# Optimization experiments

Measured on AMD Instinct MI355X. Metric: run time of the kernel, lower is better.

## Reference

```python
import jax, jax.numpy as jnp
import numpy as np

EPS = 0.1      # torchsort regularization_strength
OUTPUTS = 16   # GlobalMultimaxPool1d(outputs=16)


def _pav_decreasing(y):
    """Non-increasing isotonic regression (pool-adjacent-violators) on a 1-D array."""
    n = y.shape[0]

    def push(carry, yi):
        sums, counts, top = carry
        top = top + 1
        sums = sums.at[top].set(yi)
        counts = counts.at[top].set(1.0)

        def cond(st):
            s, c, t = st
            # mean(top) > mean(top-1)  <=>  s[t]*c[t-1] > s[t-1]*c[t]
            return (t > 0) & (s[t] * c[t - 1] > s[t - 1] * c[t])

        def merge(st):
            s, c, t = st
            s = s.at[t - 1].add(s[t]).at[t].set(0.0)
            c = c.at[t - 1].add(c[t]).at[t].set(0.0)
            return s, c, t - 1

        sums, counts, top = jax.lax.while_loop(cond, merge, (sums, counts, top))
        return (sums, counts, top), None

    init = (jnp.zeros(n, y.dtype), jnp.zeros(n, y.dtype), jnp.int32(-1))
    (sums, counts, _), _ = jax.lax.scan(push, init, y)
    means = sums / jnp.maximum(counts, 1.0)
    ends = jnp.cumsum(counts)                                 # block end offsets
    block = jnp.searchsorted(ends, jnp.arange(n) + 0.5)       # block id per position
    return means[block]


def _pav_rows(y):
    flat = y.reshape(-1, y.shape[-1])
    return jax.vmap(_pav_decreasing)(flat).reshape(y.shape)


@jax.custom_vjp
def isotonic_decreasing(y):
    return _pav_rows(y)


def _iso_fwd(y):
    v = _pav_rows(y)
    return v, v


def _iso_bwd(v, g):
    # Jacobian of PAV solution w.r.t. input is block-averaging within pooled blocks
    # (same analytic gradient torchsort uses).
    n = v.shape[-1]

    def row(vr, gr):
        new = jnp.concatenate([jnp.ones((1,), bool), vr[1:] != vr[:-1]])
        bid = jnp.cumsum(new) - 1
        s = jax.ops.segment_sum(gr, bid, num_segments=n)
        c = jax.ops.segment_sum(jnp.ones_like(gr), bid, num_segments=n)
        return (s / jnp.maximum(c, 1.0))[bid]

    gy = jax.vmap(row)(v.reshape(-1, n), g.reshape(-1, n)).reshape(v.shape)
    return (gy,)


isotonic_decreasing.defvjp(_iso_fwd, _iso_bwd)


def soft_sort(x, eps=EPS):
    """fast-soft-sort / torchsort l2 soft sort (ascending) along the last axis.

    sign=-1 (ascending): values=-x, sort descending -> s = -sort(x),
    res = isotonic_decreasing(w - s), output = -(w - res).
    """
    n = x.shape[-1]
    w = jnp.arange(n, 0, -1, dtype=x.dtype) / eps   # [n, n-1, ..., 1] / eps
    s = -jnp.sort(x, axis=-1)                        # descending sort of -x
    v = isotonic_decreasing(w - s)
    return -(w - v)


def setup_inputs() -> dict:
    key = jax.random.key(0)
    x = jax.random.normal(key, (16, 256, 2048), dtype=jnp.float32)
    return {"x": x}


def reference(x):
    z = soft_sort(x)                                  # (B, C, N) soft-ascending
    idx = z.shape[-1] - jnp.arange(OUTPUTS) - 1       # [N-1, N-2, ..., N-OUTPUTS]
    return jnp.take(z, idx, axis=-1)                  # (B, C, OUTPUTS)
```

## Files before the change

### kernel.cpp

```cpp
#include <hip/hip_runtime.h>
#include <math.h>


#define ROW_N 2048
#define K 16

__device__ __forceinline__ void ce_desc(float& a, float& b) {
    float mx = fmaxf(a, b);
    float mn = fminf(a, b);
    a = mx; b = mn;
}

__device__ __forceinline__ void sort16_desc(float* s) {
    #pragma unroll
    for (int k = 2; k <= 16; k <<= 1) {
        #pragma unroll
        for (int j = k >> 1; j > 0; j >>= 1) {
            #pragma unroll
            for (int i = 0; i < 16; ++i) {
                int l = i ^ j;
                if (l > i) {
                    if ((i & k) == 0) ce_desc(s[i], s[l]);
                    else              ce_desc(s[l], s[i]);
                }
            }
        }
    }
}

__device__ __forceinline__ void resort16_desc(float* s) {
    #pragma unroll
    for (int j = 8; j > 0; j >>= 1) {
        #pragma unroll
        for (int i = 0; i < 16; ++i) {
            int l = i ^ j;
            if (l > i) ce_desc(s[i], s[l]);
        }
    }
}

__global__ __launch_bounds__(256) void topk16_rows_kernel(
        const float* __restrict__ x, float* __restrict__ out, int nrows) {
    const int lane = threadIdx.x & 63;
    const int wid  = threadIdx.x >> 6;
    const int row  = blockIdx.x * 4 + wid;
    if (row >= nrows) return;

    const float4* rp4 = (const float4*)(x + (size_t)row * ROW_N);

    float a[16], b[16];
    #pragma unroll
    for (int j = 0; j < 4; ++j) {
        float4 t = rp4[lane + 64 * j];
        a[4 * j + 0] = t.x; a[4 * j + 1] = t.y;
        a[4 * j + 2] = t.z; a[4 * j + 3] = t.w;
    }
    #pragma unroll
    for (int j = 0; j < 4; ++j) {
        float4 t = rp4[lane + 64 * (j + 4)];
        b[4 * j + 0] = t.x; b[4 * j + 1] = t.y;
        b[4 * j + 2] = t.z; b[4 * j + 3] = t.w;
    }

    sort16_desc(a);
    sort16_desc(b);
    float t[16];
    #pragma unroll
    for (int i = 0; i < 16; ++i) t[i] = fmaxf(a[i], b[15 - i]);
    resort16_desc(t);

    #pragma unroll
    for (int st = 0; st < 6; ++st) {
        const int off = 1 << st;
        float p[16];
        #pragma unroll
        for (int i = 0; i < 16; ++i) p[i] = __shfl_xor(t[i], off, 64);
        float u[16];
        #pragma unroll
        for (int i = 0; i < 16; ++i) u[i] = fmaxf(t[i], p[15 - i]);
        resort16_desc(u);
        #pragma unroll
        for (int i = 0; i < 16; ++i) t[i] = u[i];
    }

    float myout = 0.0f;
    #pragma unroll
    for (int k = 0; k < K; ++k)
        if (lane == k) myout = t[k];
    if (lane < K) out[(size_t)row * K + lane] = myout;
}

extern "C" void kernel_launch(void* const* d_in, const int* in_sizes, int n_in,
                              void* d_out, int out_size, void* d_ws, size_t ws_size,
                              hipStream_t stream) {
    const float* x = (const float*)d_in[0];
    float* out = (float*)d_out;
    const int nrows = in_sizes[0] / ROW_N;
    const int blocks = (nrows + 3) / 4;
    topk16_rows_kernel<<<blocks, 256, 0, stream>>>(x, out, nrows);
}
```

Baseline: 15.23 us.

## Split each row across two wavefronts and merge top-16 via shared memory

Each 2048-element row is now handled by two wavefronts, each loading and sorting half the row (16 values per lane). The two per-wave top-16 lists are combined through shared memory with a bitonic merge done by shuffles. This doubles the number of waves to improve latency hiding and memory parallelism, and halves per-thread registers. It adds a __syncthreads and a small shared-memory merge, and the launch bounds now request 8 waves per EU occupancy.

```diff
diff --git a/kernel.cpp b/kernel.cpp
--- a/kernel.cpp
+++ b/kernel.cpp
@@ -2,8 +2,9 @@
 #include <math.h>
 
 
-#define ROW_N 2048
-#define K 16
+#define ROW_N  2048
+#define HALF_N 1024
+#define K      16
 
 __device__ __forceinline__ void ce_desc(float& a, float& b) {
     float mx = fmaxf(a, b);
@@ -39,55 +40,64 @@
     }
 }
 
-__global__ __launch_bounds__(256) void topk16_rows_kernel(
+__global__ __launch_bounds__(256, 8) void topk16_split_kernel(
         const float* __restrict__ x, float* __restrict__ out, int nrows) {
     const int lane = threadIdx.x & 63;
     const int wid  = threadIdx.x >> 6;
-    const int row  = blockIdx.x * 4 + wid;
-    if (row >= nrows) return;
+    const int gw   = blockIdx.x * 4 + wid;
+    int row        = gw >> 1;
+    const int half = gw & 1;
+    const bool valid = (row < nrows);
+    if (!valid) row = nrows - 1;
 
-    const float4* rp4 = (const float4*)(x + (size_t)row * ROW_N);
+    const float4* rp4 =
+        (const float4*)(x + (size_t)row * ROW_N + half * HALF_N);
 
-    float a[16], b[16];
+    float t[16];
     #pragma unroll
     for (int j = 0; j < 4; ++j) {
-        float4 t = rp4[lane + 64 * j];
-        a[4 * j + 0] = t.x; a[4 * j + 1] = t.y;
-        a[4 * j + 2] = t.z; a[4 * j + 3] = t.w;
-    }
-    #pragma unroll
-    for (int j = 0; j < 4; ++j) {
-        float4 t = rp4[lane + 64 * (j + 4)];
-        b[4 * j + 0] = t.x; b[4 * j + 1] = t.y;
-        b[4 * j + 2] = t.z; b[4 * j + 3] = t.w;
+        float4 v = rp4[lane + 64 * j];
+        t[4 * j + 0] = v.x; t[4 * j + 1] = v.y;
+        t[4 * j + 2] = v.z; t[4 * j + 3] = v.w;
     }
 
-    sort16_desc(a);
-    sort16_desc(b);
-    float t[16];
-    #pragma unroll
-    for (int i = 0; i < 16; ++i) t[i] = fmaxf(a[i], b[15 - i]);
-    resort16_desc(t);
+    sort16_desc(t);
 
     #pragma unroll
     for (int st = 0; st < 6; ++st) {
         const int off = 1 << st;
-        float p[16];
-        #pragma unroll
-        for (int i = 0; i < 16; ++i) p[i] = __shfl_xor(t[i], off, 64);
         float u[16];
         #pragma unroll
-        for (int i = 0; i < 16; ++i) u[i] = fmaxf(t[i], p[15 - i]);
+        for (int i = 0; i < 8; ++i) {
+            float pi = __shfl_xor(t[i], off, 64);
+            float pj = __shfl_xor(t[15 - i], off, 64);
+            u[i]      = fmaxf(t[i],      pj);
+            u[15 - i] = fmaxf(t[15 - i], pi);
+        }
         resort16_desc(u);
         #pragma unroll
         for (int i = 0; i < 16; ++i) t[i] = u[i];
     }
 
-    float myout = 0.0f;
+    float my = 0.0f;
     #pragma unroll
     for (int k = 0; k < K; ++k)
-        if (lane == k) myout = t[k];
-    if (lane < K) out[(size_t)row * K + lane] = myout;
+        if (lane == k) my = t[k];
+
+    __shared__ float sm[4][K];
+    if (lane < K) sm[wid][lane] = my;
+    __syncthreads();
+
+    if ((half == 0) && (lane < K)) {
+        float b = sm[wid ^ 1][(K - 1) - lane];
+        float m = fmaxf(my, b);
+        #pragma unroll
+        for (int j = 8; j >= 1; j >>= 1) {
+            float pm = __shfl_xor(m, j, 64);
+            m = ((lane & j) == 0) ? fmaxf(m, pm) : fminf(m, pm);
+        }
+        if (valid) out[(size_t)row * K + lane] = m;
+    }
 }
 
 extern "C" void kernel_launch(void* const* d_in, const int* in_sizes, int n_in,
@@ -95,7 +105,8 @@
                               hipStream_t stream) {
     const float* x = (const float*)d_in[0];
     float* out = (float*)d_out;
-    const int nrows = in_sizes[0] / ROW_N;
-    const int blocks = (nrows + 3) / 4;
-    topk16_rows_kernel<<<blocks, 256, 0, stream>>>(x, out, nrows);
+    const int nrows  = in_sizes[0] / ROW_N;
+    const int nwaves = nrows * 2;
+    const int blocks = (nwaves + 3) / 4;
+    topk16_split_kernel<<<blocks, 256, 0, stream>>>(x, out, nrows);
 }
```

Result: slower. 19.25 us (+26.4%).

## Prefilter candidates above a fixed threshold, then sort small candidate sets per row

Applied to the files above, without the earlier changes.

Replaces the full per-row bitonic top-16 with a three-pass scheme. Counters are zeroed, then a filter kernel uses ballot and atomics to gather elements above a fixed threshold into a 64-slot buffer per row. A select kernel finishes with a 64-lane shuffle sort, or falls back to the full path when the count is out of range. The goal is to avoid heavy register sorting networks, at the cost of extra launches, atomics, workspace traffic, and a threshold tuned to normally distributed inputs.

```diff
diff --git a/kernel.cpp b/kernel.cpp
--- a/kernel.cpp
+++ b/kernel.cpp
@@ -4,6 +4,9 @@
 
 #define ROW_N 2048
 #define K 16
+#define CAP 64
+#define THRESH 2.05f
+
 
 __device__ __forceinline__ void ce_desc(float& a, float& b) {
     float mx = fmaxf(a, b);
@@ -39,56 +42,148 @@
     }
 }
 
+__device__ void row_topk_full(const float* __restrict__ rp, int lane,
+                              float* t) {
+    const float4* rp4 = (const float4*)rp;
+    float a[16], b[16];
+    #pragma unroll
+    for (int j = 0; j < 4; ++j) {
+        float4 v = rp4[lane + 64 * j];
+        a[4 * j + 0] = v.x; a[4 * j + 1] = v.y;
+        a[4 * j + 2] = v.z; a[4 * j + 3] = v.w;
+    }
+    #pragma unroll
+    for (int j = 0; j < 4; ++j) {
+        float4 v = rp4[lane + 64 * (j + 4)];
+        b[4 * j + 0] = v.x; b[4 * j + 1] = v.y;
+        b[4 * j + 2] = v.z; b[4 * j + 3] = v.w;
+    }
+    sort16_desc(a);
+    sort16_desc(b);
+    #pragma unroll
+    for (int i = 0; i < 16; ++i) t[i] = fmaxf(a[i], b[15 - i]);
+    resort16_desc(t);
+    #pragma unroll
+    for (int st = 0; st < 6; ++st) {
+        const int off = 1 << st;
+        float p[16];
+        #pragma unroll
+        for (int i = 0; i < 16; ++i) p[i] = __shfl_xor(t[i], off, 64);
+        float u[16];
+        #pragma unroll
+        for (int i = 0; i < 16; ++i) u[i] = fmaxf(t[i], p[15 - i]);
+        resort16_desc(u);
+        #pragma unroll
+        for (int i = 0; i < 16; ++i) t[i] = u[i];
+    }
+}
+
+
 __global__ __launch_bounds__(256) void topk16_rows_kernel(
         const float* __restrict__ x, float* __restrict__ out, int nrows) {
     const int lane = threadIdx.x & 63;
     const int wid  = threadIdx.x >> 6;
     const int row  = blockIdx.x * 4 + wid;
     if (row >= nrows) return;
-
-    const float4* rp4 = (const float4*)(x + (size_t)row * ROW_N);
-
-    float a[16], b[16];
+    float t[16];
+    row_topk_full(x + (size_t)row * ROW_N, lane, t);
+    float my = 0.0f;
+    #pragma unroll
+    for (int k = 0; k < K; ++k)
+        if (lane == k) my = t[k];
+    if (lane < K) out[(size_t)row * K + lane] = my;
+}
+
+
+__global__ void zero_cnt_kernel(int* __restrict__ cnt, int n) {
+    int i = blockIdx.x * blockDim.x + threadIdx.x;
+    if (i < n) cnt[i] = 0;
+}
+
+
+__global__ __launch_bounds__(256, 8) void filter_kernel(
+        const float* __restrict__ x, int* __restrict__ cnt,
+        float* __restrict__ cand, int nrows) {
+    const int lane = threadIdx.x & 63;
+    const int wid  = threadIdx.x >> 6;
+    const int gw   = blockIdx.x * 4 + wid;
+    const int row  = gw >> 1;
+    const int half = gw & 1;
+    if (row >= nrows) return;
+
+    const float4* p =
+        (const float4*)(x + (size_t)row * ROW_N + half * (ROW_N / 2));
+
+    float4 v[4];
+    #pragma unroll
+    for (int j = 0; j < 4; ++j) v[j] = p[lane + 64 * j];
+
+    int*   c  = cnt + row;
+    float* cb = cand + (size_t)row * CAP;
+
     #pragma unroll
     for (int j = 0; j < 4; ++j) {
-        float4 t = rp4[lane + 64 * j];
-        a[4 * j + 0] = t.x; a[4 * j + 1] = t.y;
-        a[4 * j + 2] = t.z; a[4 * j + 3] = t.w;
-    }
-    #pragma unroll
-    for (int j = 0; j < 4; ++j) {
-        float4 t = rp4[lane + 64 * (j + 4)];
-        b[4 * j + 0] = t.x; b[4 * j + 1] = t.y;
-        b[4 * j + 2] = t.z; b[4 * j + 3] = t.w;
-    }
-
-    sort16_desc(a);
-    sort16_desc(b);
-    float t[16];
-    #pragma unroll
-    for (int i = 0; i < 16; ++i) t[i] = fmaxf(a[i], b[15 - i]);
-    resort16_desc(t);
-
-    #pragma unroll
-    for (int st = 0; st < 6; ++st) {
-        const int off = 1 << st;
-        float p[16];
-        #pragma unroll
-        for (int i = 0; i < 16; ++i) p[i] = __shfl_xor(t[i], off, 64);
-        float u[16];
-        #pragma unroll
-        for (int i = 0; i < 16; ++i) u[i] = fmaxf(t[i], p[15 - i]);
-        resort16_desc(u);
-        #pragma unroll
-        for (int i = 0; i < 16; ++i) t[i] = u[i];
-    }
-
-    float myout = 0.0f;
-    #pragma unroll
-    for (int k = 0; k < K; ++k)
-        if (lane == k) myout = t[k];
-    if (lane < K) out[(size_t)row * K + lane] = myout;
-}
+        float e0 = v[j].x, e1 = v[j].y, e2 = v[j].z, e3 = v[j].w;
+        float es[4] = {e0, e1, e2, e3};
+        #pragma unroll
+        for (int q = 0; q < 4; ++q) {
+            float e = es[q];
+            bool hit = e > THRESH;
+            unsigned long long m = __ballot(hit);
+            if (m == 0) continue;
+            int n = __popcll(m);
+            int base = 0;
+            if (lane == 0) base = atomicAdd(c, n);
+            base = __shfl(base, 0, 64);
+            if (hit) {
+                int rank = __popcll(m & ((1ull << lane) - 1ull));
+                int slot = base + rank;
+                if (slot < CAP) cb[slot] = e;
+            }
+        }
+    }
+}
+
+
+__device__ __forceinline__ float sort64_desc(float v, int lane) {
+    #pragma unroll
+    for (int k2 = 2; k2 <= 64; k2 <<= 1) {
+        #pragma unroll
+        for (int j = k2 >> 1; j >= 1; j >>= 1) {
+            float p = __shfl_xor(v, j, 64);
+            bool lower = (lane & j)  == 0;
+            bool desc  = (lane & k2) == 0;
+            float mx = fmaxf(v, p), mn = fminf(v, p);
+            v = (lower == desc) ? mx : mn;
+        }
+    }
+    return v;
+}
+
+__global__ __launch_bounds__(256) void select_kernel(
+        const float* __restrict__ x, const int* __restrict__ cnt,
+        const float* __restrict__ cand, float* __restrict__ out, int nrows) {
+    const int lane = threadIdx.x & 63;
+    const int wid  = threadIdx.x >> 6;
+    const int row  = blockIdx.x * 4 + wid;
+    if (row >= nrows) return;
+
+    const int c = cnt[row];
+    if (c >= K && c <= CAP) {
+        float v = (lane < c) ? cand[(size_t)row * CAP + lane] : -INFINITY;
+        v = sort64_desc(v, lane);
+        if (lane < K) out[(size_t)row * K + lane] = v;
+    } else {
+        float t[16];
+        row_topk_full(x + (size_t)row * ROW_N, lane, t);
+        float my = 0.0f;
+        #pragma unroll
+        for (int k = 0; k < K; ++k)
+            if (lane == k) my = t[k];
+        if (lane < K) out[(size_t)row * K + lane] = my;
+    }
+}
+
 
 extern "C" void kernel_launch(void* const* d_in, const int* in_sizes, int n_in,
                               void* d_out, int out_size, void* d_ws, size_t ws_size,
@@ -96,6 +191,18 @@
     const float* x = (const float*)d_in[0];
     float* out = (float*)d_out;
     const int nrows = in_sizes[0] / ROW_N;
-    const int blocks = (nrows + 3) / 4;
-    topk16_rows_kernel<<<blocks, 256, 0, stream>>>(x, out, nrows);
-}
+
+    const size_t cnt_bytes  = (size_t)nrows * sizeof(int);
+    const size_t cand_bytes = (size_t)nrows * CAP * sizeof(float);
+    if (ws_size < cnt_bytes + cand_bytes) {
+        topk16_rows_kernel<<<(nrows + 3) / 4, 256, 0, stream>>>(x, out, nrows);
+        return;
+    }
+
+    int*   cnt  = (int*)d_ws;
+    float* cand = (float*)((char*)d_ws + cnt_bytes);
+
+    zero_cnt_kernel<<<(nrows + 255) / 256, 256, 0, stream>>>(cnt, nrows);
+    filter_kernel<<<(nrows * 2 + 3) / 4, 256, 0, stream>>>(x, cnt, cand, nrows);
+    select_kernel<<<(nrows + 3) / 4, 256, 0, stream>>>(x, cnt, cand, out, nrows);
+}
```

Measured after the change: 28.33 us. +86.1%, slower.
